# Kernel optimization log

Measured on AMD Instinct MI355X. Metric: run time of the kernel, lower is better.

The kernel has to match this reference:

```python
import jax, jax.numpy as jnp
import numpy as np

C = 256
HEADS = 8
HEAD_DIM = C // HEADS
GROUPS = 8
EPS = 1e-5


def setup_inputs() -> dict:
    key = jax.random.key(0)
    ks = jax.random.split(key, 11)
    B, S = 2, 16
    s = 0.02
    return {
        "x": jax.random.normal(ks[0], (B, C, S, S, S), dtype=jnp.float32),
        "gn_w": jnp.ones((C,), jnp.float32),
        "gn_b": jnp.zeros((C,), jnp.float32),
        "wq": jax.random.normal(ks[1], (C, C), jnp.float32) * s,
        "bq": jnp.zeros((C,), jnp.float32),
        "wk": jax.random.normal(ks[2], (C, C), jnp.float32) * s,
        "bk": jnp.zeros((C,), jnp.float32),
        "wv": jax.random.normal(ks[3], (C, C), jnp.float32) * s,
        "bv": jnp.zeros((C,), jnp.float32),
        "wo": jax.random.normal(ks[4], (C, C), jnp.float32) * s,
        "bo": jnp.zeros((C,), jnp.float32),
    }


def _group_norm(x, w, b):
    # x: [B, C, D, H, W]; GroupNorm(8, C) with affine params
    B, Cc, D, H, W = x.shape
    xg = x.reshape(B, GROUPS, Cc // GROUPS, D, H, W)
    mu = jnp.mean(xg, axis=(2, 3, 4, 5), keepdims=True)
    var = jnp.mean(jnp.square(xg - mu), axis=(2, 3, 4, 5), keepdims=True)
    xn = ((xg - mu) * jax.lax.rsqrt(var + EPS)).reshape(B, Cc, D, H, W)
    return xn * w[None, :, None, None, None] + b[None, :, None, None, None]


def reference(x, gn_w, gn_b, wq, bq, wk, bk, wv, bv, wo, bo):
    B, Cc, D, H, W = x.shape
    N = D * H * W
    xn = _group_norm(x, gn_w, gn_b).reshape(B, Cc, N)  # [B,C,N]
    # 1x1x1 Conv3d == per-voxel linear: weight [out,in]
    Q = jnp.einsum("oc,bcn->bon", wq, xn) + bq[None, :, None]
    K = jnp.einsum("oc,bcn->bon", wk, xn) + bk[None, :, None]
    V = jnp.einsum("oc,bcn->bon", wv, xn) + bv[None, :, None]
    Q = Q.reshape(B, HEADS, HEAD_DIM, N)
    K = K.reshape(B, HEADS, HEAD_DIM, N)
    V = V.reshape(B, HEADS, HEAD_DIM, N)
    scale = np.sqrt(HEAD_DIM).astype(np.float32)
    attn = jnp.einsum("bhdn,bhdm->bhnm", Q, K) / scale
    attn = jax.nn.softmax(attn, axis=-1)
    out = jnp.einsum("bhnm,bhdm->bhdn", attn, V)  # [B,h,hd,N]
    out = out.reshape(B, Cc, N)
    out = jnp.einsum("oc,bcn->bon", wo, out) + bo[None, :, None]
    return x + out.reshape(B, Cc, D, H, W)
```

## Files before the change

### kernel.cpp

```cpp
#include <hip/hip_runtime.h>

#define B_   2
#define C_   256
#define N_   4096
#define H_   8
#define HD_  32
#define G_   8
#define CPG_ 32

typedef short short8 __attribute__((ext_vector_type(8)));
typedef short short4v __attribute__((ext_vector_type(4)));
typedef unsigned uint4v __attribute__((ext_vector_type(4)));
typedef float f32x4  __attribute__((ext_vector_type(4)));
typedef float f4     __attribute__((ext_vector_type(4)));

__device__ __forceinline__ float b2f(short s) {
    return __uint_as_float(((unsigned)(unsigned short)s) << 16);
}
__device__ __forceinline__ short f2b(float f) {
    unsigned u = __float_as_uint(f);
    unsigned r = (u + 0x7FFF + ((u >> 16) & 1)) >> 16;
    return (short)r;
}

__global__ __launch_bounds__(256) void gn_part(const float* __restrict__ x,
                                               float* __restrict__ part) {
    int blk = blockIdx.x;
    const f4* p = (const f4*)x + (size_t)(blk >> 6) * (CPG_ * N_ / 4) + (size_t)(blk & 63) * 512;
    float s = 0.f, ss = 0.f;
#pragma unroll
    for (int i = 0; i < 2; i++) {
        f4 v = p[threadIdx.x + i * 256];
#pragma unroll
        for (int j = 0; j < 4; j++) { float f = v[j]; s += f; ss += f * f; }
    }
#pragma unroll
    for (int off = 32; off > 0; off >>= 1) {
        s  += __shfl_down(s, off);
        ss += __shfl_down(ss, off);
    }
    __shared__ float rs[4], rss[4];
    int w = threadIdx.x >> 6;
    if ((threadIdx.x & 63) == 0) { rs[w] = s; rss[w] = ss; }
    __syncthreads();
    if (threadIdx.x == 0) {
        part[blk * 2]     = rs[0] + rs[1] + rs[2] + rs[3];
        part[blk * 2 + 1] = rss[0] + rss[1] + rss[2] + rss[3];
    }
}

__global__ __launch_bounds__(256) void gemm_qkv(
    const float* __restrict__ x,
    const float* __restrict__ gw, const float* __restrict__ gb,
    const float* __restrict__ part,
    const float* __restrict__ wq, const float* __restrict__ bq,
    const float* __restrict__ wk, const float* __restrict__ bk,
    const float* __restrict__ wv, const float* __restrict__ bv,
    short* __restrict__ q, short* __restrict__ kt, short* __restrict__ v) {
    int z = blockIdx.z;
    int b = z / 3, which = z % 3;
    const float* W    = which == 0 ? wq : (which == 1 ? wk : wv);
    const float* bias = which == 0 ? bq : (which == 1 ? bk : bv);
    bool trans = (which != 2);
    float mul = (which == 0) ? (0.17677669529663687f * 1.4426950408889634f) : 1.0f;

    __shared__ short wl[64][40];
    __shared__ short xl[128][40];
    __shared__ float ga[256], gbb[256];
    __shared__ float mus[8], rstds[8];

    int o0 = blockIdx.y * 64, n0 = blockIdx.x * 128;
    int tid = threadIdx.x;
    int w = tid >> 6, lane = tid & 63, li = lane & 15, quad = lane >> 4;
    int wr = w & 1, wc = w >> 1;

#pragma unroll
    for (int gi = 0; gi < 2; gi++) {
        int g = w * 2 + gi;
        const float* pp = &part[(size_t)(b * 8 + g) * 128 + lane * 2];
        float s = pp[0], ss = pp[1];
#pragma unroll
        for (int off = 32; off > 0; off >>= 1) {
            s  += __shfl_down(s, off);
            ss += __shfl_down(ss, off);
        }
        if (lane == 0) {
            const float inv = 1.f / (float)(CPG_ * N_);
            float mu = s * inv;
            float var = ss * inv - mu * mu;
            mus[g] = mu;
            rstds[g] = rsqrtf(var + 1e-5f);
        }
    }
    __syncthreads();
    {
        int c = tid, g = c >> 5;
        float a = rstds[g] * gw[c];
        ga[c]  = a;
        gbb[c] = gb[c] - mus[g] * a;
    }

    f32x4 acc[8];
#pragma unroll
    for (int i = 0; i < 8; i++) acc[i] = (f32x4){0.f, 0.f, 0.f, 0.f};

    int cpair = tid >> 4, l16 = tid & 15;
    __syncthreads();

    for (int k0 = 0; k0 < 256; k0 += 32) {
        {
            int row = tid >> 2, co = (tid & 3) << 3;
            const float* wp = &W[(size_t)(o0 + row) * 256 + k0 + co];
            f4 wa = *(const f4*)wp;
            f4 wb = *(const f4*)(wp + 4);
            short8 w8;
#pragma unroll
            for (int j = 0; j < 4; j++) { w8[j] = f2b(wa[j]); w8[j + 4] = f2b(wb[j]); }
            *(short8*)&wl[row][co] = w8;
        }
        {
            int c0 = k0 + cpair * 2;
            float a0 = ga[c0],     b0c = gbb[c0];
            float a1 = ga[c0 + 1], b1c = gbb[c0 + 1];
            const float* xr0 = x + ((size_t)(b * 256 + c0)) * N_ + n0 + l16;
            const float* xr1 = xr0 + N_;
#pragma unroll
            for (int j = 0; j < 8; j++) {
                unsigned lo = (unsigned short)f2b(xr0[16 * j] * a0 + b0c);
                unsigned hi = (unsigned short)f2b(xr1[16 * j] * a1 + b1c);
                *(unsigned*)&xl[l16 + 16 * j][cpair * 2] = lo | (hi << 16);
            }
        }
        __syncthreads();
        short8 af[4], bfr[4];
        if (trans) {
#pragma unroll
            for (int i = 0; i < 4; i++) af[i]  = *(short8*)&xl[wr * 64 + i * 16 + li][quad * 8];
#pragma unroll
            for (int j = 0; j < 2; j++) bfr[j] = *(short8*)&wl[wc * 32 + j * 16 + li][quad * 8];
#pragma unroll
            for (int i = 0; i < 4; i++)
#pragma unroll
                for (int j = 0; j < 2; j++)
                    acc[i * 2 + j] = __builtin_amdgcn_mfma_f32_16x16x32_bf16(af[i], bfr[j], acc[i * 2 + j], 0, 0, 0);
        } else {
#pragma unroll
            for (int i = 0; i < 2; i++) af[i]  = *(short8*)&wl[wr * 32 + i * 16 + li][quad * 8];
#pragma unroll
            for (int j = 0; j < 4; j++) bfr[j] = *(short8*)&xl[wc * 64 + j * 16 + li][quad * 8];
#pragma unroll
            for (int i = 0; i < 2; i++)
#pragma unroll
                for (int j = 0; j < 4; j++)
                    acc[i * 4 + j] = __builtin_amdgcn_mfma_f32_16x16x32_bf16(af[i], bfr[j], acc[i * 4 + j], 0, 0, 0);
        }
        __syncthreads();
    }

    if (which == 2) {
        short* outp = v + (size_t)b * C_ * N_;
#pragma unroll
        for (int i = 0; i < 2; i++) {
            int ob = o0 + wr * 32 + i * 16 + quad * 4;
#pragma unroll
            for (int j = 0; j < 4; j++) {
                int n_ = n0 + wc * 64 + j * 16 + li;
#pragma unroll
                for (int r = 0; r < 4; r++) {
                    float val = acc[i * 4 + j][r] + bias[ob + r];
                    outp[(size_t)(ob + r) * N_ + n_] = f2b(val);
                }
            }
        }
    } else if (which == 0) {
        short* outp = q + (size_t)b * N_ * C_;
#pragma unroll
        for (int i = 0; i < 4; i++) {
            int nb_ = n0 + wr * 64 + i * 16 + quad * 4;
#pragma unroll
            for (int j = 0; j < 2; j++) {
                int o_ = o0 + wc * 32 + j * 16 + li;
                float bv_ = bias[o_];
#pragma unroll
                for (int r = 0; r < 4; r++)
                    outp[(size_t)(nb_ + r) * C_ + o_] = f2b((acc[i * 2 + j][r] + bv_) * mul);
            }
        }
    } else {
#pragma unroll
        for (int i = 0; i < 4; i++) {
            int nb_ = n0 + wr * 64 + i * 16 + quad * 4;
#pragma unroll
            for (int j = 0; j < 2; j++) {
                int o_ = o0 + wc * 32 + j * 16 + li;
                int hh = o_ >> 5, d = o_ & 31;
                float bv_ = bias[o_];
                short* kdst = kt + ((size_t)(b * 8 + hh) * N_) * HD_ + d;
#pragma unroll
                for (int r = 0; r < 4; r++)
                    kdst[(size_t)(nb_ + r) * HD_] = f2b(acc[i * 2 + j][r] + bv_);
            }
        }
    }
}

__global__ __launch_bounds__(512) void flash(const short* __restrict__ q,
                                             const short* __restrict__ ktp,
                                             const short* __restrict__ v,
                                             short* __restrict__ aoT) {
    int bid = blockIdx.x;
    int xcd = bid & 7;
    int s_  = bid >> 3;
    int bh  = xcd * 2 + (s_ & 1);
    int nb  = s_ >> 1;
    int b = bh >> 3, h = bh & 7;

    const short* QT = q   + (size_t)b * N_ * C_ + h * HD_;
    const short* KP = ktp + (size_t)bh * N_ * HD_;
    const short* V  = v   + ((size_t)b * C_ + h * HD_) * N_;
    short* O = aoT + (size_t)b * N_ * C_ + h * HD_;

    __shared__ short kl[2 * 2560];
    __shared__ short vl[2 * 2304];

    int tid = threadIdx.x, w = tid >> 6, lane = tid & 63, li = lane & 15, quad = lane >> 4;
    int n0w = nb * 128 + w * 16;

    short8 qf0 = *(const short8*)&QT[(size_t)(n0w + li) * 256 + quad * 8];

    f32x4 oa00 = (f32x4){0.f,0.f,0.f,0.f}, oa01 = oa00;
    float lr0 = 0.f;
    const f32x4 zero = (f32x4){0.f, 0.f, 0.f, 0.f};

    int krow = tid >> 3, kcol = (tid & 7) << 2;
    const short* kgp = KP + (size_t)krow * HD_ + kcol;
    int klo = krow * 40 + kcol;
    int vd = tid >> 4, g = tid & 15;
    int mbase = 32 * (g >> 3) + 16 * (g & 1) + 4 * ((g >> 1) & 3);
    const short* vgp = V + (size_t)vd * N_ + mbase;
    int vlo = vd * 72 + g * 4;

    short4v kst = *(const short4v*)kgp;
    short4v vst = *(const short4v*)vgp;

    f32x4 s0[4];
    short8 vf[4];

    for (int t = 0; t < 64; ++t) {
        int buf = t & 1;
        *(short4v*)&kl[buf * 2560 + klo] = kst;
        *(short4v*)&vl[buf * 2304 + vlo] = vst;
        if (t < 63) {
            kst = *(const short4v*)(kgp + (size_t)(t + 1) * 64 * HD_);
            vst = *(const short4v*)(vgp + (t + 1) * 64);
        }
        __syncthreads();

        __builtin_amdgcn_s_setprio(1);
#pragma unroll
        for (int c = 0; c < 4; c++) {
            short8 kf = *(short8*)&kl[buf * 2560 + (c * 16 + li) * 40 + quad * 8];
            s0[c] = __builtin_amdgcn_mfma_f32_16x16x32_bf16(kf, qf0, zero, 0, 0, 0);
        }
        __builtin_amdgcn_s_setprio(0);

        vf[0] = *(short8*)&vl[buf * 2304 + li * 72 + quad * 8];
        vf[1] = *(short8*)&vl[buf * 2304 + (16 + li) * 72 + quad * 8];
        vf[2] = *(short8*)&vl[buf * 2304 + li * 72 + 32 + quad * 8];
        vf[3] = *(short8*)&vl[buf * 2304 + (16 + li) * 72 + 32 + quad * 8];

        unsigned paw[8];
        float lp = 0.f;
#pragma unroll
        for (int c = 0; c < 4; c++) {
            float e0 = __builtin_amdgcn_exp2f(s0[c][0]);
            float e1 = __builtin_amdgcn_exp2f(s0[c][1]);
            float e2 = __builtin_amdgcn_exp2f(s0[c][2]);
            float e3 = __builtin_amdgcn_exp2f(s0[c][3]);
            lp += (e0 + e1) + (e2 + e3);
            paw[2 * c]     = __builtin_amdgcn_perm(__float_as_uint(e1), __float_as_uint(e0), 0x07060302);
            paw[2 * c + 1] = __builtin_amdgcn_perm(__float_as_uint(e3), __float_as_uint(e2), 0x07060302);
        }
        lr0 += lp;
        uint4v p0 = (uint4v){paw[0], paw[1], paw[2], paw[3]};
        uint4v p1 = (uint4v){paw[4], paw[5], paw[6], paw[7]};
        short8 af0 = __builtin_bit_cast(short8, p0);
        short8 af1 = __builtin_bit_cast(short8, p1);

        __builtin_amdgcn_s_setprio(1);
        oa00 = __builtin_amdgcn_mfma_f32_16x16x32_bf16(af0, vf[0], oa00, 0, 0, 0);
        oa01 = __builtin_amdgcn_mfma_f32_16x16x32_bf16(af0, vf[1], oa01, 0, 0, 0);
        oa00 = __builtin_amdgcn_mfma_f32_16x16x32_bf16(af1, vf[2], oa00, 0, 0, 0);
        oa01 = __builtin_amdgcn_mfma_f32_16x16x32_bf16(af1, vf[3], oa01, 0, 0, 0);
        __builtin_amdgcn_s_setprio(0);
    }

    lr0 += __shfl_xor(lr0, 16); lr0 += __shfl_xor(lr0, 32);
#pragma unroll
    for (int r2 = 0; r2 < 4; r2++) {
        float ln0 = __shfl(lr0, quad * 4 + r2);
        float inv0 = 1.f / ln0;
        size_t n_ = (size_t)(n0w + quad * 4 + r2);
        O[n_ * 256 + li]      = f2b(oa00[r2] * inv0);
        O[n_ * 256 + 16 + li] = f2b(oa01[r2] * inv0);
    }
}

__global__ __launch_bounds__(256) void gemm_out(const float* __restrict__ W,
                                                const float* __restrict__ bias,
                                                const short* __restrict__ aoT,
                                                const float* __restrict__ resid,
                                                float* __restrict__ out) {
    int b = blockIdx.z;
    const short* X = aoT + (size_t)b * N_ * C_;
    const float* R = resid + (size_t)b * C_ * N_;
    float* outp = out + (size_t)b * C_ * N_;

    __shared__ short wl[128][40];
    __shared__ short xl[64][40];

    int o0 = blockIdx.y * 128, n0 = blockIdx.x * 64;
    int tid = threadIdx.x;
    int w = tid >> 6, lane = tid & 63, li = lane & 15, quad = lane >> 4;
    int wr = w & 1, wc = w >> 1;

    f32x4 acc[4][2];
#pragma unroll
    for (int i = 0; i < 4; i++)
#pragma unroll
        for (int j = 0; j < 2; j++) acc[i][j] = (f32x4){0.f, 0.f, 0.f, 0.f};

    for (int k0 = 0; k0 < 256; k0 += 32) {
#pragma unroll
        for (int i = 0; i < 2; i++) {
            int idx = tid + i * 256;
            int row = idx >> 2, co = (idx & 3) << 3;
            const float* wp = &W[(size_t)(o0 + row) * 256 + k0 + co];
            f4 wa = *(const f4*)wp;
            f4 wb = *(const f4*)(wp + 4);
            short8 w8;
#pragma unroll
            for (int j = 0; j < 4; j++) { w8[j] = f2b(wa[j]); w8[j + 4] = f2b(wb[j]); }
            *(short8*)&wl[row][co] = w8;
        }
        {
            int row = tid >> 2, co = (tid & 3) << 3;
            *(short8*)&xl[row][co] = *(const short8*)&X[(size_t)(n0 + row) * 256 + k0 + co];
        }
        __syncthreads();
        short8 af[4], bfr[2];
#pragma unroll
        for (int i = 0; i < 4; i++) af[i]  = *(short8*)&wl[wr * 64 + i * 16 + li][quad * 8];
#pragma unroll
        for (int j = 0; j < 2; j++) bfr[j] = *(short8*)&xl[wc * 32 + j * 16 + li][quad * 8];
#pragma unroll
        for (int i = 0; i < 4; i++)
#pragma unroll
            for (int j = 0; j < 2; j++)
                acc[i][j] = __builtin_amdgcn_mfma_f32_16x16x32_bf16(af[i], bfr[j], acc[i][j], 0, 0, 0);
        __syncthreads();
    }
#pragma unroll
    for (int i = 0; i < 4; i++) {
        int ob = o0 + wr * 64 + i * 16 + quad * 4;
#pragma unroll
        for (int j = 0; j < 2; j++) {
            int n_ = n0 + wc * 32 + j * 16 + li;
#pragma unroll
            for (int r = 0; r < 4; r++) {
                size_t idx = (size_t)(ob + r) * N_ + n_;
                outp[idx] = acc[i][j][r] + bias[ob + r] + R[idx];
            }
        }
    }
}

extern "C" void kernel_launch(void* const* d_in, const int* in_sizes, int n_in,
                              void* d_out, int out_size, void* d_ws, size_t ws_size,
                              hipStream_t stream) {
    const float* x  = (const float*)d_in[0];
    const float* gw = (const float*)d_in[1];
    const float* gb = (const float*)d_in[2];
    const float* wq = (const float*)d_in[3];
    const float* bq = (const float*)d_in[4];
    const float* wk = (const float*)d_in[5];
    const float* bk = (const float*)d_in[6];
    const float* wv = (const float*)d_in[7];
    const float* bv = (const float*)d_in[8];
    const float* wo = (const float*)d_in[9];
    const float* bo = (const float*)d_in[10];
    float* out = (float*)d_out;

    char* ws = (char*)d_ws;
    float* part = (float*)ws;
    const size_t TS = (size_t)B_ * N_ * C_;
    short* aoT = (short*)(ws + 16384);
    short* q   = aoT + TS;
    short* kt  = q + TS;
    short* v   = kt + TS;

    gn_part<<<1024, 256, 0, stream>>>(x, part);
    gemm_qkv<<<dim3(32, 4, 6), 256, 0, stream>>>(x, gw, gb, part,
                                                 wq, bq, wk, bk, wv, bv, q, kt, v);
    flash<<<512, 512, 0, stream>>>(q, kt, v, aoT);
    gemm_out<<<dim3(64, 2, 2), 256, 0, stream>>>(wo, bo, aoT, x, out);
}
```

Before: 155.5 us.

## Split flash attention over KV halves with doubled query rows per wave and combine kernel

Each wave now processes 32 query rows instead of 16, so every K/V tile loaded into shared memory is reused by twice as many MFMAs. The KV sequence is split into two halves across blocks, which keeps the block count at 512. Each block writes unnormalized fp32 partial outputs and row sums, and a new combine kernel adds the halves, normalizes and converts to bf16. This trades extra global traffic for the fp32 partials and an additional kernel launch against fewer K/V loads per unit of compute. Because the softmax has no max subtraction, partials can be summed directly.

```diff
diff --git a/kernel.cpp b/kernel.cpp
--- a/kernel.cpp
+++ b/kernel.cpp
@@ -207,29 +207,34 @@
 __global__ __launch_bounds__(512) void flash(const short* __restrict__ q,
                                              const short* __restrict__ ktp,
                                              const short* __restrict__ v,
-                                             short* __restrict__ aoT) {
+                                             float* __restrict__ Opart,
+                                             float* __restrict__ lrbuf) {
     int bid = blockIdx.x;
     int xcd = bid & 7;
-    int s_  = bid >> 3;
-    int bh  = xcd * 2 + (s_ & 1);
-    int nb  = s_ >> 1;
+    int rest = bid >> 3;
+    int bh = xcd * 2 + (rest & 1);
+    int r2 = rest >> 1;
+    int nb = r2 & 15;
+    int half = r2 >> 4;
     int b = bh >> 3, h = bh & 7;
 
     const short* QT = q   + (size_t)b * N_ * C_ + h * HD_;
-    const short* KP = ktp + (size_t)bh * N_ * HD_;
-    const short* V  = v   + ((size_t)b * C_ + h * HD_) * N_;
-    short* O = aoT + (size_t)b * N_ * C_ + h * HD_;
+    const short* KP = ktp + (size_t)bh * N_ * HD_ + (size_t)half * 2048 * HD_;
+    const short* V  = v   + ((size_t)b * C_ + h * HD_) * N_ + half * 2048;
+    float* Oh  = Opart + (size_t)half * B_ * N_ * C_ + (size_t)b * N_ * C_ + h * HD_;
+    float* lrp = lrbuf + (size_t)half * 16 * N_ + (size_t)bh * N_;
 
     __shared__ short kl[2 * 2560];
     __shared__ short vl[2 * 2304];
 
     int tid = threadIdx.x, w = tid >> 6, lane = tid & 63, li = lane & 15, quad = lane >> 4;
-    int n0w = nb * 128 + w * 16;
+    int n0w = nb * 256 + w * 32;
 
     short8 qf0 = *(const short8*)&QT[(size_t)(n0w + li) * 256 + quad * 8];
-
-    f32x4 oa00 = (f32x4){0.f,0.f,0.f,0.f}, oa01 = oa00;
-    float lr0 = 0.f;
+    short8 qf1 = *(const short8*)&QT[(size_t)(n0w + 16 + li) * 256 + quad * 8];
+
+    f32x4 oa00 = (f32x4){0.f,0.f,0.f,0.f}, oa01 = oa00, oa10 = oa00, oa11 = oa00;
+    float lr0 = 0.f, lr1 = 0.f;
     const f32x4 zero = (f32x4){0.f, 0.f, 0.f, 0.f};
 
     int krow = tid >> 3, kcol = (tid & 7) << 2;
@@ -243,14 +248,14 @@
     short4v kst = *(const short4v*)kgp;
     short4v vst = *(const short4v*)vgp;
 
-    f32x4 s0[4];
+    f32x4 s0[4], s1[4];
     short8 vf[4];
 
-    for (int t = 0; t < 64; ++t) {
+    for (int t = 0; t < 32; ++t) {
         int buf = t & 1;
         *(short4v*)&kl[buf * 2560 + klo] = kst;
         *(short4v*)&vl[buf * 2304 + vlo] = vst;
-        if (t < 63) {
+        if (t < 31) {
             kst = *(const short4v*)(kgp + (size_t)(t + 1) * 64 * HD_);
             vst = *(const short4v*)(vgp + (t + 1) * 64);
         }
@@ -261,6 +266,7 @@
         for (int c = 0; c < 4; c++) {
             short8 kf = *(short8*)&kl[buf * 2560 + (c * 16 + li) * 40 + quad * 8];
             s0[c] = __builtin_amdgcn_mfma_f32_16x16x32_bf16(kf, qf0, zero, 0, 0, 0);
+            s1[c] = __builtin_amdgcn_mfma_f32_16x16x32_bf16(kf, qf1, zero, 0, 0, 0);
         }
         __builtin_amdgcn_s_setprio(0);
 
@@ -284,26 +290,78 @@
         lr0 += lp;
         uint4v p0 = (uint4v){paw[0], paw[1], paw[2], paw[3]};
         uint4v p1 = (uint4v){paw[4], paw[5], paw[6], paw[7]};
-        short8 af0 = __builtin_bit_cast(short8, p0);
-        short8 af1 = __builtin_bit_cast(short8, p1);
+        short8 a0 = __builtin_bit_cast(short8, p0);
+        short8 a1 = __builtin_bit_cast(short8, p1);
+
+        lp = 0.f;
+#pragma unroll
+        for (int c = 0; c < 4; c++) {
+            float e0 = __builtin_amdgcn_exp2f(s1[c][0]);
+            float e1 = __builtin_amdgcn_exp2f(s1[c][1]);
+            float e2 = __builtin_amdgcn_exp2f(s1[c][2]);
+            float e3 = __builtin_amdgcn_exp2f(s1[c][3]);
+            lp += (e0 + e1) + (e2 + e3);
+            paw[2 * c]     = __builtin_amdgcn_perm(__float_as_uint(e1), __float_as_uint(e0), 0x07060302);
+            paw[2 * c + 1] = __builtin_amdgcn_perm(__float_as_uint(e3), __float_as_uint(e2), 0x07060302);
+        }
+        lr1 += lp;
+        uint4v p2 = (uint4v){paw[0], paw[1], paw[2], paw[3]};
+        uint4v p3 = (uint4v){paw[4], paw[5], paw[6], paw[7]};
+        short8 a2 = __builtin_bit_cast(short8, p2);
+        short8 a3 = __builtin_bit_cast(short8, p3);
 
         __builtin_amdgcn_s_setprio(1);
-        oa00 = __builtin_amdgcn_mfma_f32_16x16x32_bf16(af0, vf[0], oa00, 0, 0, 0);
-        oa01 = __builtin_amdgcn_mfma_f32_16x16x32_bf16(af0, vf[1], oa01, 0, 0, 0);
-        oa00 = __builtin_amdgcn_mfma_f32_16x16x32_bf16(af1, vf[2], oa00, 0, 0, 0);
-        oa01 = __builtin_amdgcn_mfma_f32_16x16x32_bf16(af1, vf[3], oa01, 0, 0, 0);
+        oa00 = __builtin_amdgcn_mfma_f32_16x16x32_bf16(a0, vf[0], oa00, 0, 0, 0);
+        oa01 = __builtin_amdgcn_mfma_f32_16x16x32_bf16(a0, vf[1], oa01, 0, 0, 0);
+        oa00 = __builtin_amdgcn_mfma_f32_16x16x32_bf16(a1, vf[2], oa00, 0, 0, 0);
+        oa01 = __builtin_amdgcn_mfma_f32_16x16x32_bf16(a1, vf[3], oa01, 0, 0, 0);
+        oa10 = __builtin_amdgcn_mfma_f32_16x16x32_bf16(a2, vf[0], oa10, 0, 0, 0);
+        oa11 = __builtin_amdgcn_mfma_f32_16x16x32_bf16(a2, vf[1], oa11, 0, 0, 0);
+        oa10 = __builtin_amdgcn_mfma_f32_16x16x32_bf16(a3, vf[2], oa10, 0, 0, 0);
+        oa11 = __builtin_amdgcn_mfma_f32_16x16x32_bf16(a3, vf[3], oa11, 0, 0, 0);
         __builtin_amdgcn_s_setprio(0);
     }
 
     lr0 += __shfl_xor(lr0, 16); lr0 += __shfl_xor(lr0, 32);
-#pragma unroll
-    for (int r2 = 0; r2 < 4; r2++) {
-        float ln0 = __shfl(lr0, quad * 4 + r2);
-        float inv0 = 1.f / ln0;
-        size_t n_ = (size_t)(n0w + quad * 4 + r2);
-        O[n_ * 256 + li]      = f2b(oa00[r2] * inv0);
-        O[n_ * 256 + 16 + li] = f2b(oa01[r2] * inv0);
-    }
+    lr1 += __shfl_xor(lr1, 16); lr1 += __shfl_xor(lr1, 32);
+#pragma unroll
+    for (int r = 0; r < 4; r++) {
+        size_t n_ = (size_t)(n0w + quad * 4 + r);
+        Oh[n_ * 256 + li]      = oa00[r];
+        Oh[n_ * 256 + 16 + li] = oa01[r];
+        size_t n2 = (size_t)(n0w + 16 + quad * 4 + r);
+        Oh[n2 * 256 + li]      = oa10[r];
+        Oh[n2 * 256 + 16 + li] = oa11[r];
+    }
+    if (quad == 0) {
+        lrp[n0w + li]      = lr0;
+        lrp[n0w + 16 + li] = lr1;
+    }
+}
+
+__global__ __launch_bounds__(256) void combine(const float* __restrict__ Opart,
+                                               const float* __restrict__ lrbuf,
+                                               short* __restrict__ aoT) {
+    int idx = blockIdx.x * 256 + threadIdx.x;
+    int cg = idx & 31;
+    int n  = (idx >> 5) & 4095;
+    int b  = idx >> 17;
+    int c0 = cg * 8;
+    int bh = b * 8 + (c0 >> 5);
+    float l = lrbuf[(size_t)bh * N_ + n] + lrbuf[(size_t)16 * N_ + (size_t)bh * N_ + n];
+    float inv = 1.f / l;
+    size_t base = ((size_t)b * N_ + n) * 256 + c0;
+    const float* p0 = Opart + base;
+    const float* p1 = Opart + (size_t)B_ * N_ * C_ + base;
+    f4 x0 = *(const f4*)p0, x1 = *(const f4*)(p0 + 4);
+    f4 y0 = *(const f4*)p1, y1 = *(const f4*)(p1 + 4);
+    short8 r;
+#pragma unroll
+    for (int j = 0; j < 4; j++) {
+        r[j]     = f2b((x0[j] + y0[j]) * inv);
+        r[j + 4] = f2b((x1[j] + y1[j]) * inv);
+    }
+    *(short8*)&aoT[base] = r;
 }
 
 __global__ __launch_bounds__(256) void gemm_out(const float* __restrict__ W,
@@ -398,10 +456,13 @@
     short* q   = aoT + TS;
     short* kt  = q + TS;
     short* v   = kt + TS;
+    float* Of  = (float*)(v + TS);
+    float* lr  = Of + 2 * TS;
 
     gn_part<<<1024, 256, 0, stream>>>(x, part);
     gemm_qkv<<<dim3(32, 4, 6), 256, 0, stream>>>(x, gw, gb, part,
                                                  wq, bq, wk, bk, wv, bv, q, kt, v);
-    flash<<<512, 512, 0, stream>>>(q, kt, v, aoT);
+    flash<<<512, 512, 0, stream>>>(q, kt, v, Of, lr);
+    combine<<<1024, 256, 0, stream>>>(Of, lr, aoT);
     gemm_out<<<dim3(64, 2, 2), 256, 0, stream>>>(wo, bo, aoT, x, out);
 }
```

Measured after the change: 149.8 us. 3.6% less time.
